# Optimization experiments

Measured on AMD Instinct MI355X. Metric: run time of the kernel, lower is better.

## Reference

```python
import jax, jax.numpy as jnp
import numpy as np

# ---- static geometry derived from truncation (matches torch __init__) ----
T = 127
N_LAT_NH = T + 1                                   # 128 NH latitudes
LONS = [20 + 4 * i for i in range(N_LAT_NH)]       # octahedral reduced grid
CUMS = np.concatenate([[0], np.cumsum(np.array(LONS + LONS[::-1]))]).astype(int)
HZW_NH = np.minimum(4 + np.arange(N_LAT_NH), T)    # cubic truncation: m_max = nlon//4 - 1, capped at T
N_LATS_PER_M = np.array([(HZW_NH >= m).sum() for m in range(T + 1)])
L_SYM_FULL = (T + 3) // 2                          # 65 rows before dropping row 0
L_ANT = (T + 2) // 2                               # 64
N_VARS = 128
BATCH, ENS = 4, 1


def _tri_masks():
    """Zero-padded triangular structure of the per-m Legendre matrices."""
    sym = np.zeros((T + 1, L_SYM_FULL, N_LAT_NH), np.float32)
    ant = np.zeros((T + 1, L_ANT, N_LAT_NH), np.float32)
    for m in range(T + 1):
        n_lats = int(N_LATS_PER_M[m])
        ms = (T - m + 3) // 2
        off = L_SYM_FULL - ms
        sym[m, off:, N_LAT_NH - n_lats:] = 1.0
        if (m + 1) % 2 == 1:
            sym[m, off, :] = 0.0
        ma = (T - m + 2) // 2
        off = L_ANT - ma
        ant[m, off:, N_LAT_NH - n_lats:] = 1.0
        if m % 2 == 1:
            ant[m, off, :] = 0.0
    return sym[:, 1:, :], ant   # module drops first symmetric row -> [128,64,128]


def setup_inputs() -> dict:
    key = jax.random.key(0)
    k1, k2, k3 = jax.random.split(key, 3)
    n_grid = int(CUMS[-1])
    x = jax.random.normal(k1, (BATCH, ENS, n_grid, N_VARS), jnp.float32)
    sm, am = _tri_masks()
    # random stand-ins for (gaussian-weight-fused) Legendre polynomials, with the exact
    # triangular zero structure the module builds from ecTrans assets
    symmetric = jax.random.normal(k2, sm.shape, jnp.float32) * jnp.asarray(sm)
    antisymmetric = jax.random.normal(k3, am.shape, jnp.float32) * jnp.asarray(am)
    return {"x": x, "symmetric": symmetric, "antisymmetric": antisymmetric}


def reference(x, symmetric, antisymmetric):
    """Octahedral SHT forward: ragged longitudinal rfft -> hemispheric fold -> per-m Legendre matmuls.

    Returns spectrum [b, e, l, m, vars, 2] (real/imag stacked on last axis).
    """
    n_lat = 2 * N_LAT_NH
    north, south = [], []
    # loop is over structurally distinct (ragged) latitude ring lengths; NH lat i and its
    # SH mirror (lat n_lat-1-i) share nlon/truncation, so batch them in one FFT call.
    for i in range(N_LAT_NH):
        j = n_lat - 1 - i
        nlon = LONS[i]
        xn = x[:, :, CUMS[i]:CUMS[i + 1], :]           # [b,e,nlon,v]
        xs = x[:, :, CUMS[j]:CUMS[j + 1], :]
        xp = jnp.stack([xn, xs], axis=2)               # [b,e,2,nlon,v]
        f = jnp.fft.rfft(xp, axis=3) / nlon            # torch norm='forward'
        m_hi = int(HZW_NH[i]) + 1                      # keep m <= highest zonal wavenumber
        f = f[:, :, :, :m_hi, :]
        f = jnp.pad(f, ((0, 0), (0, 0), (0, 0), (0, T + 1 - m_hi), (0, 0)))
        north.append(f[:, :, 0])
        south.append(f[:, :, 1])                       # index i <-> lat n_lat-1-i: already pole-mirrored
    north = jnp.stack(north, axis=2)                   # [b,e,n_lat_nh,m,v] complex64
    south = jnp.stack(south, axis=2)
    # hemispheric symmetry of Legendre polynomials
    sym = north + south
    anti = north - south
    # per-m truncated Legendre contractions over NH latitudes (n)
    out_s = jnp.einsum('mln,benmv->belmv', symmetric, sym)     # [b,e,64,m,v]
    out_a = jnp.einsum('mln,benmv->belmv', antisymmetric, anti)
    # interleave symmetric (l-m even) and antisymmetric (l-m odd) rows -> full l axis (128)
    spec = jnp.stack([out_s, out_a], axis=3)
    b, e, L, _, M, V = spec.shape
    spec = spec.reshape(b, e, 2 * L, M, V)             # [b,e,l,m,v] complex, lower triangle zeros
    return jnp.stack([spec.real, spec.imag], axis=-1)  # real view [b,e,l,m,v,2]
```

## Files before the change

kernel.cpp:

```cpp
#include <hip/hip_runtime.h>
#include <hip/hip_bf16.h>

#define NGRID 70144
#define NV 128

typedef float f32x4 __attribute__((ext_vector_type(4)));
typedef short short8 __attribute__((ext_vector_type(8)));

__device__ __forceinline__ unsigned f2bf(float f){
  return (unsigned)__bfloat16_as_ushort(__float2bfloat16(f));
}
__device__ __forceinline__ float bf2f(unsigned h){ return __uint_as_float(h<<16); }
__device__ __forceinline__ unsigned packsplit(float f){
  unsigned h = f2bf(f);
  unsigned l = f2bf(f - bf2f(h));
  return (h<<16) | l;
}
__device__ __forceinline__ int swzc(int c){ return (c ^ (c>>3)) & 7; }

__device__ __forceinline__ void unpack_frag(int4 a, int4 b, short8 &bh, short8 &bl){
  int h0 = (int)(((unsigned)a.x >> 16) | ((unsigned)a.y & 0xFFFF0000u));
  int h1 = (int)(((unsigned)a.z >> 16) | ((unsigned)a.w & 0xFFFF0000u));
  int h2 = (int)(((unsigned)b.x >> 16) | ((unsigned)b.y & 0xFFFF0000u));
  int h3 = (int)(((unsigned)b.z >> 16) | ((unsigned)b.w & 0xFFFF0000u));
  int l0 = (int)(((unsigned)a.x & 0xFFFFu) | ((unsigned)a.y << 16));
  int l1 = (int)(((unsigned)a.z & 0xFFFFu) | ((unsigned)a.w << 16));
  int l2 = (int)(((unsigned)b.x & 0xFFFFu) | ((unsigned)b.y << 16));
  int l3 = (int)(((unsigned)b.z & 0xFFFFu) | ((unsigned)b.w << 16));
  int4 H = make_int4(h0,h1,h2,h3), L = make_int4(l0,l1,l2,l3);
  bh = *(short8*)&H; bl = *(short8*)&L;
}

struct TileT { unsigned char ring, mc, type, vh; };
constexpr int nvar_of(int r){
  int mhi=(5+r<128)?(5+r):128;
  int mtn=(mhi+15)/16;
  int nch=(mtn+3)/4;
  return nch*4;
}
constexpr int calc_ntiles(){
  int tot=0;
  for(int g=0; g<16; g++){
    int mv=0;
    for(int q=0;q<8;q++){ int nv=nvar_of(127-(g*8+q)); if(nv>mv) mv=nv; }
    tot += 8*mv;
  }
  return tot;
}
constexpr int NTILES = calc_ntiles();
struct Tiles { TileT t[NTILES]; };
constexpr Tiles make_tiles(){
  Tiles T{}; int k=0;
  for(int g=0; g<16; g++){
    int mv=0;
    for(int q=0;q<8;q++){ int nv=nvar_of(127-(g*8+q)); if(nv>mv) mv=nv; }
    for(int var=0; var<mv; var++)
      for(int q=0;q<8;q++){
        int r = 127-(g*8+q);
        if(var < nvar_of(r)){
          T.t[k].ring=(unsigned char)r;
          T.t[k].mc  =(unsigned char)(var>>2);
          T.t[k].type=(unsigned char)((var>>1)&1);
          T.t[k].vh  =(unsigned char)(var&1);
        } else {
          T.t[k].ring=255;
        }
        k++;
      }
  }
  return T;
}
__constant__ Tiles TILES = make_tiles();

struct Offs { long o[129]; };
constexpr Offs make_offs(){
  Offs O{}; long off=0;
  for(int r=0;r<128;r++){
    O.o[r]=off;
    int mh=(5+r<128)?(5+r):128, jc=11+2*r;
    off += 4L*(((mh+15)/16)*16)*(((jc+31)/32)*32);
  }
  O.o[128]=off;
  return O;
}
__constant__ Offs TWOFF = make_offs();
constexpr long TWATOT = make_offs().o[128];

__global__ void fill_tw(unsigned short* __restrict__ twA){
  int ring = blockIdx.x, t = blockIdx.y, mq = blockIdx.z;
  int N = 20+4*ring, H = N/2, JC = H+1;
  int mhi = (5+ring<128)?(5+ring):128;
  int Mpad = ((mhi+15)>>4)<<4;
  int Kpad = ((JC+31)>>5)<<5;
  long MK = (long)Mpad*Kpad;
  unsigned short* hiT = twA + TWOFF.o[ring] + (long)(t*2)*MK;
  unsigned short* loT = hiT + MK;
  float invN = 1.0f/(float)N;
  int tid = threadIdx.x;
  for(int m=mq; m<Mpad; m+=4){
    int p0   = (int)(((long)m*tid) % N);
    int step = (int)(((long)m*256) % N);
    int p = p0;
    for(int j=tid;j<Kpad;j+=256){
      float val = 0.f;
      if(m < mhi && j < JC){
        float th = 6.2831853071795864f * (float)p * invN;
        float sn, cs; __sincosf(th,&sn,&cs);
        val = (t ? -sn : cs) * invN;
      }
      unsigned h = f2bf(val);
      unsigned l = f2bf(val - bf2f(h));
      long idx = (long)m*Kpad + j;
      hiT[idx] = (unsigned short)h;
      loT[idx] = (unsigned short)l;
      p += step; if(p>=N) p-=N;
    }
  }
}

__global__ __launch_bounds__(256) void dft_mfma(const float* __restrict__ x,
                                                const unsigned short* __restrict__ twA,
                                                unsigned* __restrict__ Gp){
  TileT tl = TILES.t[blockIdx.x];
  if(tl.ring == 255) return;
  int ring = tl.ring, type = tl.type, vh = tl.vh;
  int b = blockIdx.y;
  int N = 20+4*ring, H = N/2, JC = H+1;
  int mhi = (5+ring<128)?(5+ring):128;
  int MtN = (mhi+15)>>4;
  int Mt0 = tl.mc*4;
  int KT = (JC+31)>>5;
  int Kpad = KT<<5;
  int Mpad = MtN<<4;

  long MK = (long)Mpad*Kpad;
  const unsigned short* Ahi = twA + TWOFF.o[ring] + (long)(type*2)*MK;
  const unsigned short* Alo = Ahi + MK;

  const float* xn = x + ((long)b*NGRID + (long)ring*(2*ring+18))*NV;
  long a1 = ring+1;
  const float* xs = x + ((long)b*NGRID + (NGRID - a1*(2*a1+18)))*NV;

  __shared__ __align__(16) unsigned Bp[4096];

  int tid = threadIdx.x;
  int jb = tid >> 5;
  int vp = tid & 31;
  int vo = vh*64 + vp*2;
  int wave = tid >> 6, lane = tid & 63;
  int jj = lane & 15, kb = lane >> 4;

  f32x4 acc[4][2];
  #pragma unroll
  for(int Mt=0;Mt<4;Mt++){ acc[Mt][0]=(f32x4){0.f,0.f,0.f,0.f}; acc[Mt][1]=(f32x4){0.f,0.f,0.f,0.f}; }

  for(int kt=0; kt<KT; ++kt){
    __syncthreads();
    float gSx[4], gSy[4], gAx[4], gAy[4];
    #pragma unroll
    for(int dj=0;dj<4;dj++){
      int j = kt*32 + jb*4 + dj;
      float2 nj=make_float2(0.f,0.f), sj=nj, np=nj, sp=nj;
      if(j < JC){
        nj = *(const float2*)&xn[(long)j*NV + vo];
        sj = *(const float2*)&xs[(long)j*NV + vo];
        if(j > 0 && j < H){
          int jp = N - j;
          np = *(const float2*)&xn[(long)jp*NV + vo];
          sp = *(const float2*)&xs[(long)jp*NV + vo];
        }
      }
      float ex=nj.x+sj.x, ey=nj.y+sj.y, ox=nj.x-sj.x, oy=nj.y-sj.y;
      float epx=np.x+sp.x, epy=np.y+sp.y, opx=np.x-sp.x, opy=np.y-sp.y;
      gSx[dj] = type ? (ex-epx) : (ex+epx);
      gSy[dj] = type ? (ey-epy) : (ey+epy);
      gAx[dj] = type ? (ox-opx) : (ox+opx);
      gAy[dj] = type ? (oy-opy) : (oy+opy);
    }
    {
      int c0 = (vp*2)*2;
      int4 w0 = make_int4((int)packsplit(gSx[0]),(int)packsplit(gSx[1]),
                          (int)packsplit(gSx[2]),(int)packsplit(gSx[3]));
      *(int4*)&Bp[c0*32 + ((jb*4) ^ (swzc(c0)<<2))] = w0;
      int c1 = c0+1;
      int4 w1 = make_int4((int)packsplit(gAx[0]),(int)packsplit(gAx[1]),
                          (int)packsplit(gAx[2]),(int)packsplit(gAx[3]));
      *(int4*)&Bp[c1*32 + ((jb*4) ^ (swzc(c1)<<2))] = w1;
      int c2 = c0+2;
      int4 w2 = make_int4((int)packsplit(gSy[0]),(int)packsplit(gSy[1]),
                          (int)packsplit(gSy[2]),(int)packsplit(gSy[3]));
      *(int4*)&Bp[c2*32 + ((jb*4) ^ (swzc(c2)<<2))] = w2;
      int c3 = c0+3;
      int4 w3 = make_int4((int)packsplit(gAy[0]),(int)packsplit(gAy[1]),
                          (int)packsplit(gAy[2]),(int)packsplit(gAy[3]));
      *(int4*)&Bp[c3*32 + ((jb*4) ^ (swzc(c3)<<2))] = w3;
    }
    __syncthreads();
    short8 bh[2], bl[2];
    #pragma unroll
    for(int ct=0;ct<2;ct++){
      int c = wave*32 + ct*16 + jj;
      int sw = swzc(c)<<2;
      int4 pa = *(const int4*)&Bp[c*32 + ((kb*8) ^ sw)];
      int4 pb = *(const int4*)&Bp[c*32 + ((kb*8+4) ^ sw)];
      unpack_frag(pa, pb, bh[ct], bl[ct]);
    }
    #pragma unroll
    for(int Mt=0;Mt<4;Mt++){
      if(Mt0+Mt < MtN){
        long ao = (long)((Mt0+Mt)*16 + jj)*Kpad + kt*32 + kb*8;
        short8 ah = *(const short8*)&Ahi[ao];
        short8 al = *(const short8*)&Alo[ao];
        #pragma unroll
        for(int ct=0;ct<2;ct++){
          acc[Mt][ct] = __builtin_amdgcn_mfma_f32_16x16x32_bf16(ah, bh[ct], acc[Mt][ct], 0,0,0);
          acc[Mt][ct] = __builtin_amdgcn_mfma_f32_16x16x32_bf16(al, bh[ct], acc[Mt][ct], 0,0,0);
          acc[Mt][ct] = __builtin_amdgcn_mfma_f32_16x16x32_bf16(ah, bl[ct], acc[Mt][ct], 0,0,0);
        }
      }
    }
  }
  #pragma unroll
  for(int Mt=0;Mt<4;Mt++){
    if(Mt0+Mt < MtN){
      #pragma unroll
      for(int ct=0;ct<2;ct++){
        int cg = vh*128 + wave*32 + ct*16 + jj;
        int s = cg & 1, v = cg >> 1;
        #pragma unroll
        for(int reg=0;reg<4;reg++){
          int m = (Mt0+Mt)*16 + (kb<<2) + reg;
          if(m < mhi){
            Gp[(long)((s*2+type)*128 + m)*65536 + (long)ring*512 + b*128 + v]
              = packsplit(acc[Mt][ct][reg]);
          }
        }
      }
    }
  }
}

__global__ void w_split(const float* __restrict__ Wsym, const float* __restrict__ Want,
                        unsigned short* __restrict__ Wh, unsigned short* __restrict__ Wl){
  long i = (long)blockIdx.x*256 + threadIdx.x;
  const float* W = (i < 1048576) ? Wsym : Want;
  float w = W[i & 1048575];
  unsigned h = f2bf(w);
  unsigned l = f2bf(w - bf2f(h));
  Wh[i] = (unsigned short)h;
  Wl[i] = (unsigned short)l;
}

__global__ __launch_bounds__(256) void legendre_mfma(const unsigned short* __restrict__ Wh,
                                                     const unsigned short* __restrict__ Wl,
                                                     const unsigned* __restrict__ Gp,
                                                     float* __restrict__ out){
  int m = blockIdx.x, b = blockIdx.y, s = blockIdx.z;
  __shared__ __align__(16) unsigned Bp[8192];
  int tid = threadIdx.x;
  int wave = tid >> 6, lane = tid & 63;
  int jj = lane & 15, kb = lane >> 4;

  int kt0 = (m > 4) ? ((m-4) >> 5) : 0;

  const unsigned short* WA = Wh + (long)(s*128+m)*8192;
  const unsigned short* WB = Wl + (long)(s*128+m)*8192;
  int ri = tid & 1, v = tid >> 1;
  long gC0 = (long)((s*2+ri)*128 + m)*65536 + (long)b*128 + v;

  f32x4 acc[4][4];
  #pragma unroll
  for(int a=0;a<4;a++)
    #pragma unroll
    for(int q=0;q<4;q++) acc[a][q] = (f32x4){0.f,0.f,0.f,0.f};

  int swT = swzc(tid)<<2;
  for(int kt=kt0; kt<4; ++kt){
    __syncthreads();
    #pragma unroll
    for(int k4=0;k4<32;k4+=4){
      int4 w = make_int4((int)Gp[gC0 + (long)(kt*32+k4+0)*512],
                         (int)Gp[gC0 + (long)(kt*32+k4+1)*512],
                         (int)Gp[gC0 + (long)(kt*32+k4+2)*512],
                         (int)Gp[gC0 + (long)(kt*32+k4+3)*512]);
      *(int4*)&Bp[tid*32 + (k4 ^ swT)] = w;
    }
    __syncthreads();
    short8 bh[4], bl[4];
    #pragma unroll
    for(int nt=0;nt<4;nt++){
      int c = (wave*4+nt)*16 + jj;
      int sw = swzc(c)<<2;
      int4 pa = *(const int4*)&Bp[c*32 + ((kb*8) ^ sw)];
      int4 pb = *(const int4*)&Bp[c*32 + ((kb*8+4) ^ sw)];
      unpack_frag(pa, pb, bh[nt], bl[nt]);
    }
    #pragma unroll
    for(int Mt=0;Mt<4;Mt++){
      long ao = (long)(Mt*16 + jj)*128 + kt*32 + kb*8;
      short8 ah = *(const short8*)&WA[ao];
      short8 al = *(const short8*)&WB[ao];
      #pragma unroll
      for(int nt=0;nt<4;nt++){
        acc[Mt][nt] = __builtin_amdgcn_mfma_f32_16x16x32_bf16(ah, bh[nt], acc[Mt][nt], 0,0,0);
        acc[Mt][nt] = __builtin_amdgcn_mfma_f32_16x16x32_bf16(al, bh[nt], acc[Mt][nt], 0,0,0);
        acc[Mt][nt] = __builtin_amdgcn_mfma_f32_16x16x32_bf16(ah, bl[nt], acc[Mt][nt], 0,0,0);
      }
    }
  }
  int r4 = (lane>>4)<<2;
  #pragma unroll
  for(int Mt=0;Mt<4;Mt++){
    #pragma unroll
    for(int nt=0;nt<4;nt++){
      int c = (wave*4+nt)*16 + jj;
      #pragma unroll
      for(int reg=0;reg<4;reg++){
        int l = Mt*16 + r4 + reg;
        out[((long)(b*128 + 2*l + s)*128 + m)*256 + c] = acc[Mt][nt][reg];
      }
    }
  }
}

extern "C" void kernel_launch(void* const* d_in, const int* in_sizes, int n_in,
                              void* d_out, int out_size, void* d_ws, size_t ws_size,
                              hipStream_t stream) {
  const float* x    = (const float*)d_in[0];
  const float* Wsym = (const float*)d_in[1];
  const float* Want = (const float*)d_in[2];
  float* out = (float*)d_out;

  size_t gpOffB = (size_t)TWATOT*2;
  if(gpOffB < 8388608) gpOffB = 8388608;
  gpOffB = (gpOffB + 255) & ~(size_t)255;

  unsigned short* twA = (unsigned short*)d_ws;
  unsigned* Gp = (unsigned*)((char*)d_ws + gpOffB);
  unsigned short* Wh = (unsigned short*)d_ws;
  unsigned short* Wl = Wh + 2097152;

  hipLaunchKernelGGL(fill_tw,       dim3(128,2,4),   dim3(256), 0, stream, twA);
  hipLaunchKernelGGL(dft_mfma,      dim3(NTILES,4),  dim3(256), 0, stream, x, twA, Gp);
  hipLaunchKernelGGL(w_split,       dim3(8192),      dim3(256), 0, stream, Wsym, Want, Wh, Wl);
  hipLaunchKernelGGL(legendre_mfma, dim3(128,4,2),   dim3(256), 0, stream, Wh, Wl, Gp, out);
}
```

Before: 358.8 us.

## Cover all m-tiles per DFT block and prefetch next x slice into registers

Removes the split over m-chunks so each dft_mfma block computes all up to 8 m-tiles for its ring/type/vh. The input x is then loaded and folded once per block instead of once per chunk. The global loads for the next k-step are issued before the MFMA phase to hide their latency, and launch bounds now request 3 blocks per SM. The cost is a larger accumulator array (8x2 f32x4) with more register pressure and fewer blocks, which lowers parallelism for small rings.

```diff
diff --git a/kernel.cpp b/kernel.cpp
--- a/kernel.cpp
+++ b/kernel.cpp
@@ -31,40 +31,18 @@
   bh = *(short8*)&H; bl = *(short8*)&L;
 }
 
-struct TileT { unsigned char ring, mc, type, vh; };
-constexpr int nvar_of(int r){
-  int mhi=(5+r<128)?(5+r):128;
-  int mtn=(mhi+15)/16;
-  int nch=(mtn+3)/4;
-  return nch*4;
-}
-constexpr int calc_ntiles(){
-  int tot=0;
-  for(int g=0; g<16; g++){
-    int mv=0;
-    for(int q=0;q<8;q++){ int nv=nvar_of(127-(g*8+q)); if(nv>mv) mv=nv; }
-    tot += 8*mv;
-  }
-  return tot;
-}
-constexpr int NTILES = calc_ntiles();
+struct TileT { unsigned char ring, type, vh; };
+constexpr int NTILES = 512;
 struct Tiles { TileT t[NTILES]; };
 constexpr Tiles make_tiles(){
   Tiles T{}; int k=0;
   for(int g=0; g<16; g++){
-    int mv=0;
-    for(int q=0;q<8;q++){ int nv=nvar_of(127-(g*8+q)); if(nv>mv) mv=nv; }
-    for(int var=0; var<mv; var++)
-      for(int q=0;q<8;q++){
+    for(int var=0; var<4; var++)
+      for(int q=0; q<8; q++){
         int r = 127-(g*8+q);
-        if(var < nvar_of(r)){
-          T.t[k].ring=(unsigned char)r;
-          T.t[k].mc  =(unsigned char)(var>>2);
-          T.t[k].type=(unsigned char)((var>>1)&1);
-          T.t[k].vh  =(unsigned char)(var&1);
-        } else {
-          T.t[k].ring=255;
-        }
+        T.t[k].ring=(unsigned char)r;
+        T.t[k].type=(unsigned char)(var>>1);
+        T.t[k].vh  =(unsigned char)(var&1);
         k++;
       }
   }
@@ -118,17 +96,15 @@
   }
 }
 
-__global__ __launch_bounds__(256) void dft_mfma(const float* __restrict__ x,
-                                                const unsigned short* __restrict__ twA,
-                                                unsigned* __restrict__ Gp){
+__global__ __launch_bounds__(256,3) void dft_mfma(const float* __restrict__ x,
+                                                  const unsigned short* __restrict__ twA,
+                                                  unsigned* __restrict__ Gp){
   TileT tl = TILES.t[blockIdx.x];
-  if(tl.ring == 255) return;
   int ring = tl.ring, type = tl.type, vh = tl.vh;
   int b = blockIdx.y;
   int N = 20+4*ring, H = N/2, JC = H+1;
   int mhi = (5+ring<128)?(5+ring):128;
   int MtN = (mhi+15)>>4;
-  int Mt0 = tl.mc*4;
   int KT = (JC+31)>>5;
   int Kpad = KT<<5;
   int Mpad = MtN<<4;
@@ -150,52 +126,66 @@
   int wave = tid >> 6, lane = tid & 63;
   int jj = lane & 15, kb = lane >> 4;
 
-  f32x4 acc[4][2];
+  f32x4 acc[8][2];
   #pragma unroll
-  for(int Mt=0;Mt<4;Mt++){ acc[Mt][0]=(f32x4){0.f,0.f,0.f,0.f}; acc[Mt][1]=(f32x4){0.f,0.f,0.f,0.f}; }
-
+  for(int Mt=0;Mt<8;Mt++){ acc[Mt][0]=(f32x4){0.f,0.f,0.f,0.f}; acc[Mt][1]=(f32x4){0.f,0.f,0.f,0.f}; }
+
+  float2 rn[4], rs[4], rpn[4], rps[4];
+  #define LOADX(KT_)                                              \
+  {                                                               \
+    int ktl = (KT_);                                              \
+    _Pragma("unroll")                                             \
+    for(int dj=0;dj<4;dj++){                                      \
+      int j = ktl*32 + jb*4 + dj;                                 \
+      float2 zz = make_float2(0.f,0.f);                           \
+      rn[dj]=zz; rs[dj]=zz; rpn[dj]=zz; rps[dj]=zz;               \
+      if(j < JC){                                                 \
+        rn[dj] = *(const float2*)&xn[(long)j*NV + vo];            \
+        rs[dj] = *(const float2*)&xs[(long)j*NV + vo];            \
+        if(j > 0 && j < H){                                       \
+          int jp = N - j;                                         \
+          rpn[dj] = *(const float2*)&xn[(long)jp*NV + vo];        \
+          rps[dj] = *(const float2*)&xs[(long)jp*NV + vo];        \
+        }                                                         \
+      }                                                           \
+    }                                                             \
+  }
+
+  LOADX(0);
   for(int kt=0; kt<KT; ++kt){
+    int4 w0, w1, w2, w3;
+    {
+      float sx[4], sy[4], ax[4], ay[4];
+      #pragma unroll
+      for(int dj=0;dj<4;dj++){
+        float ex=rn[dj].x+rs[dj].x, ey=rn[dj].y+rs[dj].y;
+        float ox=rn[dj].x-rs[dj].x, oy=rn[dj].y-rs[dj].y;
+        float epx=rpn[dj].x+rps[dj].x, epy=rpn[dj].y+rps[dj].y;
+        float opx=rpn[dj].x-rps[dj].x, opy=rpn[dj].y-rps[dj].y;
+        sx[dj] = type ? (ex-epx) : (ex+epx);
+        sy[dj] = type ? (ey-epy) : (ey+epy);
+        ax[dj] = type ? (ox-opx) : (ox+opx);
+        ay[dj] = type ? (oy-opy) : (oy+opy);
+      }
+      w0 = make_int4((int)packsplit(sx[0]),(int)packsplit(sx[1]),
+                     (int)packsplit(sx[2]),(int)packsplit(sx[3]));
+      w1 = make_int4((int)packsplit(ax[0]),(int)packsplit(ax[1]),
+                     (int)packsplit(ax[2]),(int)packsplit(ax[3]));
+      w2 = make_int4((int)packsplit(sy[0]),(int)packsplit(sy[1]),
+                     (int)packsplit(sy[2]),(int)packsplit(sy[3]));
+      w3 = make_int4((int)packsplit(ay[0]),(int)packsplit(ay[1]),
+                     (int)packsplit(ay[2]),(int)packsplit(ay[3]));
+    }
     __syncthreads();
-    float gSx[4], gSy[4], gAx[4], gAy[4];
-    #pragma unroll
-    for(int dj=0;dj<4;dj++){
-      int j = kt*32 + jb*4 + dj;
-      float2 nj=make_float2(0.f,0.f), sj=nj, np=nj, sp=nj;
-      if(j < JC){
-        nj = *(const float2*)&xn[(long)j*NV + vo];
-        sj = *(const float2*)&xs[(long)j*NV + vo];
-        if(j > 0 && j < H){
-          int jp = N - j;
-          np = *(const float2*)&xn[(long)jp*NV + vo];
-          sp = *(const float2*)&xs[(long)jp*NV + vo];
-        }
-      }
-      float ex=nj.x+sj.x, ey=nj.y+sj.y, ox=nj.x-sj.x, oy=nj.y-sj.y;
-      float epx=np.x+sp.x, epy=np.y+sp.y, opx=np.x-sp.x, opy=np.y-sp.y;
-      gSx[dj] = type ? (ex-epx) : (ex+epx);
-      gSy[dj] = type ? (ey-epy) : (ey+epy);
-      gAx[dj] = type ? (ox-opx) : (ox+opx);
-      gAy[dj] = type ? (oy-opy) : (oy+opy);
-    }
     {
-      int c0 = (vp*2)*2;
-      int4 w0 = make_int4((int)packsplit(gSx[0]),(int)packsplit(gSx[1]),
-                          (int)packsplit(gSx[2]),(int)packsplit(gSx[3]));
-      *(int4*)&Bp[c0*32 + ((jb*4) ^ (swzc(c0)<<2))] = w0;
-      int c1 = c0+1;
-      int4 w1 = make_int4((int)packsplit(gAx[0]),(int)packsplit(gAx[1]),
-                          (int)packsplit(gAx[2]),(int)packsplit(gAx[3]));
-      *(int4*)&Bp[c1*32 + ((jb*4) ^ (swzc(c1)<<2))] = w1;
-      int c2 = c0+2;
-      int4 w2 = make_int4((int)packsplit(gSy[0]),(int)packsplit(gSy[1]),
-                          (int)packsplit(gSy[2]),(int)packsplit(gSy[3]));
-      *(int4*)&Bp[c2*32 + ((jb*4) ^ (swzc(c2)<<2))] = w2;
-      int c3 = c0+3;
-      int4 w3 = make_int4((int)packsplit(gAy[0]),(int)packsplit(gAy[1]),
-                          (int)packsplit(gAy[2]),(int)packsplit(gAy[3]));
-      *(int4*)&Bp[c3*32 + ((jb*4) ^ (swzc(c3)<<2))] = w3;
+      int c0 = vp*4;
+      *(int4*)&Bp[(c0+0)*32 + ((jb*4) ^ (swzc(c0+0)<<2))] = w0;
+      *(int4*)&Bp[(c0+1)*32 + ((jb*4) ^ (swzc(c0+1)<<2))] = w1;
+      *(int4*)&Bp[(c0+2)*32 + ((jb*4) ^ (swzc(c0+2)<<2))] = w2;
+      *(int4*)&Bp[(c0+3)*32 + ((jb*4) ^ (swzc(c0+3)<<2))] = w3;
     }
     __syncthreads();
+    if(kt+1 < KT) LOADX(kt+1);
     short8 bh[2], bl[2];
     #pragma unroll
     for(int ct=0;ct<2;ct++){
@@ -206,9 +196,9 @@
       unpack_frag(pa, pb, bh[ct], bl[ct]);
     }
     #pragma unroll
-    for(int Mt=0;Mt<4;Mt++){
-      if(Mt0+Mt < MtN){
-        long ao = (long)((Mt0+Mt)*16 + jj)*Kpad + kt*32 + kb*8;
+    for(int Mt=0;Mt<8;Mt++){
+      if(Mt < MtN){
+        long ao = (long)(Mt*16 + jj)*Kpad + kt*32 + kb*8;
         short8 ah = *(const short8*)&Ahi[ao];
         short8 al = *(const short8*)&Alo[ao];
         #pragma unroll
@@ -221,15 +211,15 @@
     }
   }
   #pragma unroll
-  for(int Mt=0;Mt<4;Mt++){
-    if(Mt0+Mt < MtN){
+  for(int Mt=0;Mt<8;Mt++){
+    if(Mt < MtN){
       #pragma unroll
       for(int ct=0;ct<2;ct++){
         int cg = vh*128 + wave*32 + ct*16 + jj;
         int s = cg & 1, v = cg >> 1;
         #pragma unroll
         for(int reg=0;reg<4;reg++){
-          int m = (Mt0+Mt)*16 + (kb<<2) + reg;
+          int m = Mt*16 + (kb<<2) + reg;
           if(m < mhi){
             Gp[(long)((s*2+type)*128 + m)*65536 + (long)ring*512 + b*128 + v]
               = packsplit(acc[Mt][ct][reg]);
@@ -238,6 +228,7 @@
       }
     }
   }
+  #undef LOADX
 }
 
 __global__ void w_split(const float* __restrict__ Wsym, const float* __restrict__ Want,
```

Result: no change. 357.7 us (-0.3%).
